# Kernel optimization log

Measured on AMD Instinct MI355X. Metric: run time of the kernel, lower is better.

## Reference

```python
import jax, jax.numpy as jnp
import numpy as np

N_NODES = 500_000
MEM_D = 128
MSG_D = 256  # stored messages have MSG_D + 1 columns (message + timestamp slot)
B = 200_000


def setup_inputs() -> dict:
    key = jax.random.key(0)
    k1, k2, k3, k4, k5, k6, k7 = jax.random.split(key, 7)
    memory = jax.random.normal(k1, (N_NODES, MEM_D), dtype=jnp.float32)
    last_update = jax.random.uniform(k2, (N_NODES,), dtype=jnp.float32)
    messages = jax.random.normal(k3, (N_NODES, MSG_D + 1), dtype=jnp.float32)
    node_id_to_messages = jax.random.normal(k4, (N_NODES, MSG_D + 1), dtype=jnp.float32)
    values = jax.random.normal(k5, (B, MEM_D), dtype=jnp.float32)
    node_idxs = jax.random.randint(k6, (B,), 0, N_NODES, dtype=jnp.int64 if jax.config.jax_enable_x64 else jnp.int32)
    nodes = jax.random.randint(k7, (B,), 0, N_NODES, dtype=jnp.int64 if jax.config.jax_enable_x64 else jnp.int32)
    return {
        "memory": memory,
        "last_update": last_update,
        "messages": messages,
        "node_id_to_messages": node_id_to_messages,
        "values": values,
        "node_idxs": node_idxs,
        "nodes": nodes,
    }


def reference(memory, last_update, messages, node_id_to_messages, values, node_idxs, nodes):
    # get_memory: row gather from persistent memory buffer
    mem_out = memory[node_idxs]                      # [B, MEM_D]
    # get_last_update: scalar gather
    lu_out = last_update[node_idxs]                  # [B]
    # set_memory: row scatter (index_copy) into memory buffer
    new_memory = memory.at[node_idxs].set(values)    # [N, MEM_D]
    # store_raw_messages: messages[nodes, :] = node_id_to_messages[nodes]
    new_messages = messages.at[nodes].set(node_id_to_messages[nodes])  # [N, MSG_D+1]
    return mem_out, lu_out, new_memory, new_messages
```

## Files before the change

### kernel.cpp

```cpp
#include <hip/hip_runtime.h>

#define N_NODES 500000
#define MEM_D   128
#define MSG_W   257
#define BATCH   200000

#define G_UNITS   6400000
#define M_UNITS   16000000
#define S_UNITS   32125000
#define GM_UNITS  22400000
#define TOTAL_UNITS 54525000

typedef float f4 __attribute__((ext_vector_type(4)));

__device__ __forceinline__ f4 nt_load4(const f4* p) {
    return __builtin_nontemporal_load(p);
}
__device__ __forceinline__ void nt_store4(f4* p, f4 v) {
    __builtin_nontemporal_store(v, p);
}

__global__ void init_kernel(int* __restrict__ winner,
                            unsigned int* __restrict__ flag32) {
    int i = blockIdx.x * blockDim.x + threadIdx.x;
    int stride = gridDim.x * blockDim.x;
    for (int j = i; j < N_NODES; j += stride) winner[j] = -1;
    for (int j = i; j < N_NODES / 4; j += stride) flag32[j] = 0u;
}

__global__ void scatter_idx_kernel(const int* __restrict__ node_idxs,
                                   const int* __restrict__ nodes,
                                   int* __restrict__ winner,
                                   unsigned char* __restrict__ flag) {
    int i = blockIdx.x * blockDim.x + threadIdx.x;
    int stride = gridDim.x * blockDim.x;
    for (; i < BATCH; i += stride) {
        atomicMax(&winner[node_idxs[i]], i);
        flag[nodes[i]] = 1;
    }
}

__global__ void fused_kernel(const float* __restrict__ memory,
                             const float* __restrict__ last_update,
                             const float* __restrict__ messages,
                             const float* __restrict__ nid2msg,
                             const float* __restrict__ values,
                             const int* __restrict__ node_idxs,
                             const int* __restrict__ winner,
                             const unsigned char* __restrict__ flag,
                             float* __restrict__ mem_out,
                             float* __restrict__ lu_out,
                             float* __restrict__ new_memory,
                             float* __restrict__ new_messages) {
    const f4* mem4 = reinterpret_cast<const f4*>(memory);
    const f4* val4 = reinterpret_cast<const f4*>(values);
    const f4* msg4 = reinterpret_cast<const f4*>(messages);
    const f4* src4 = reinterpret_cast<const f4*>(nid2msg);
    f4* memout4 = reinterpret_cast<f4*>(mem_out);
    f4* newmem4 = reinterpret_cast<f4*>(new_memory);
    f4* newmsg4 = reinterpret_cast<f4*>(new_messages);

    int i = blockIdx.x * blockDim.x + threadIdx.x;
    int stride = gridDim.x * blockDim.x;
    for (; i < TOTAL_UNITS; i += stride) {
        if (i < G_UNITS) {
            int row  = i >> 5;
            int col4 = i & 31;
            int idx  = node_idxs[row];
            f4 v = mem4[(long)idx * 32 + col4];
            nt_store4(&memout4[i], v);
            if (col4 == 0) {
                __builtin_nontemporal_store(last_update[idx], &lu_out[row]);
            }
        } else if (i < GM_UNITS) {
            int j    = i - G_UNITS;
            int row  = j >> 5;
            int col4 = j & 31;
            int w = winner[row];
            f4 v;
            if (w >= 0) {
                v = val4[(long)w * 32 + col4];
            } else {
                v = nt_load4(&mem4[j]);
            }
            nt_store4(&newmem4[j], v);
        } else {
            int j = i - GM_UNITS;
            int e  = j * 4;
            int r0 = e / 257;
            int r3 = (e + 3) / 257;
            if (r0 == r3) {
                f4 v;
                if (flag[r0]) {
                    v = nt_load4(&src4[j]);
                } else {
                    v = nt_load4(&msg4[j]);
                }
                nt_store4(&newmsg4[j], v);
            } else {
                #pragma unroll
                for (int k = 0; k < 4; ++k) {
                    int r = (e + k) / 257;
                    float v = (flag[r] ? nid2msg : messages)[e + k];
                    new_messages[e + k] = v;
                }
            }
        }
    }
}

extern "C" void kernel_launch(void* const* d_in, const int* in_sizes, int n_in,
                              void* d_out, int out_size, void* d_ws, size_t ws_size,
                              hipStream_t stream) {
    const float* memory       = (const float*)d_in[0];
    const float* last_update  = (const float*)d_in[1];
    const float* messages     = (const float*)d_in[2];
    const float* nid2msg      = (const float*)d_in[3];
    const float* values       = (const float*)d_in[4];
    const int*   node_idxs    = (const int*)d_in[5];
    const int*   nodes        = (const int*)d_in[6];

    float* out = (float*)d_out;
    float* mem_out      = out;
    float* lu_out       = out + (long)BATCH * MEM_D;
    float* new_memory   = lu_out + BATCH;
    float* new_messages = new_memory + (long)N_NODES * MEM_D;

    int* winner = (int*)d_ws;
    unsigned char* flag = (unsigned char*)d_ws + (size_t)N_NODES * sizeof(int);

    const int BS = 256;

    init_kernel<<<512, BS, 0, stream>>>(winner, (unsigned int*)flag);

    scatter_idx_kernel<<<(BATCH + BS - 1) / BS, BS, 0, stream>>>(
        node_idxs, nodes, winner, flag);

    fused_kernel<<<2048, BS, 0, stream>>>(memory, last_update, messages,
                                          nid2msg, values, node_idxs,
                                          winner, flag,
                                          mem_out, lu_out, new_memory,
                                          new_messages);
}
```

Baseline: 360.7 us.

## Split fused kernel into per-segment loops with 4-way unrolled batched loads

Replaces the single unified grid-stride loop, which branched per unit across three segments, with separate loops for the gather, memory scatter and message copy. Each loop issues four independent 16-byte loads before storing them, giving more memory-level parallelism per thread. The last_update gather moves into its own loop over batch rows. The cost is more registers per thread and extra tail-loop code.

Result: slower. 392.5 us (+8.8%).

```diff
diff --git a/kernel.cpp b/kernel.cpp
--- a/kernel.cpp
+++ b/kernel.cpp
@@ -5,11 +5,9 @@
 #define MSG_W   257
 #define BATCH   200000
 
-#define G_UNITS   6400000
-#define M_UNITS   16000000
-#define S_UNITS   32125000
-#define GM_UNITS  22400000
-#define TOTAL_UNITS 54525000
+#define G_UNITS 6400000
+#define M_UNITS 16000000
+#define S_UNITS 32125000
 
 typedef float f4 __attribute__((ext_vector_type(4)));
 
@@ -60,49 +58,101 @@
     f4* newmem4 = reinterpret_cast<f4*>(new_memory);
     f4* newmsg4 = reinterpret_cast<f4*>(new_messages);
 
-    int i = blockIdx.x * blockDim.x + threadIdx.x;
-    int stride = gridDim.x * blockDim.x;
-    for (; i < TOTAL_UNITS; i += stride) {
-        if (i < G_UNITS) {
-            int row  = i >> 5;
-            int col4 = i & 31;
-            int idx  = node_idxs[row];
-            f4 v = mem4[(long)idx * 32 + col4];
-            nt_store4(&memout4[i], v);
-            if (col4 == 0) {
-                __builtin_nontemporal_store(last_update[idx], &lu_out[row]);
+    const int tid = blockIdx.x * blockDim.x + threadIdx.x;
+    const int stride = gridDim.x * blockDim.x;
+
+    for (int r = tid; r < BATCH; r += stride) {
+        __builtin_nontemporal_store(last_update[node_idxs[r]], &lu_out[r]);
+    }
+
+    {
+        int i = tid;
+        for (; i + 3 * stride < G_UNITS; i += 4 * stride) {
+            f4 v[4];
+            #pragma unroll
+            for (int u = 0; u < 4; ++u) {
+                int ii = i + u * stride;
+                int idx = node_idxs[ii >> 5];
+                v[u] = mem4[(long)idx * 32 + (ii & 31)];
             }
-        } else if (i < GM_UNITS) {
-            int j    = i - G_UNITS;
-            int row  = j >> 5;
-            int col4 = j & 31;
-            int w = winner[row];
+            #pragma unroll
+            for (int u = 0; u < 4; ++u) nt_store4(&memout4[i + u * stride], v[u]);
+        }
+        for (; i < G_UNITS; i += stride) {
+            int idx = node_idxs[i >> 5];
+            nt_store4(&memout4[i], mem4[(long)idx * 32 + (i & 31)]);
+        }
+    }
+
+    {
+        int i = tid;
+        for (; i + 3 * stride < M_UNITS; i += 4 * stride) {
+            f4 v[4];
+            #pragma unroll
+            for (int u = 0; u < 4; ++u) {
+                int ii = i + u * stride;
+                int w = winner[ii >> 5];
+                if (w >= 0) v[u] = val4[(long)w * 32 + (ii & 31)];
+                else        v[u] = nt_load4(&mem4[ii]);
+            }
+            #pragma unroll
+            for (int u = 0; u < 4; ++u) nt_store4(&newmem4[i + u * stride], v[u]);
+        }
+        for (; i < M_UNITS; i += stride) {
+            int w = winner[i >> 5];
             f4 v;
-            if (w >= 0) {
-                v = val4[(long)w * 32 + col4];
-            } else {
-                v = nt_load4(&mem4[j]);
+            if (w >= 0) v = val4[(long)w * 32 + (i & 31)];
+            else        v = nt_load4(&mem4[i]);
+            nt_store4(&newmem4[i], v);
+        }
+    }
+
+    {
+        int i = tid;
+        for (; i + 3 * stride < S_UNITS; i += 4 * stride) {
+            f4 v[4];
+            int bnd[4];
+            #pragma unroll
+            for (int u = 0; u < 4; ++u) {
+                int ii = i + u * stride;
+                int e  = ii * 4;
+                int r0 = e / 257;
+                int r3 = (e + 3) / 257;
+                bnd[u] = (r0 != r3);
+                if (!bnd[u]) {
+                    if (flag[r0]) v[u] = nt_load4(&src4[ii]);
+                    else          v[u] = nt_load4(&msg4[ii]);
+                }
             }
-            nt_store4(&newmem4[j], v);
-        } else {
-            int j = i - GM_UNITS;
-            int e  = j * 4;
+            #pragma unroll
+            for (int u = 0; u < 4; ++u) {
+                int ii = i + u * stride;
+                if (!bnd[u]) {
+                    nt_store4(&newmsg4[ii], v[u]);
+                } else {
+                    int e = ii * 4;
+                    #pragma unroll
+                    for (int k = 0; k < 4; ++k) {
+                        int r = (e + k) / 257;
+                        new_messages[e + k] = (flag[r] ? nid2msg : messages)[e + k];
+                    }
+                }
+            }
+        }
+        for (; i < S_UNITS; i += stride) {
+            int e  = i * 4;
             int r0 = e / 257;
             int r3 = (e + 3) / 257;
             if (r0 == r3) {
                 f4 v;
-                if (flag[r0]) {
-                    v = nt_load4(&src4[j]);
-                } else {
-                    v = nt_load4(&msg4[j]);
-                }
-                nt_store4(&newmsg4[j], v);
+                if (flag[r0]) v = nt_load4(&src4[i]);
+                else          v = nt_load4(&msg4[i]);
+                nt_store4(&newmsg4[i], v);
             } else {
                 #pragma unroll
                 for (int k = 0; k < 4; ++k) {
                     int r = (e + k) / 257;
-                    float v = (flag[r] ? nid2msg : messages)[e + k];
-                    new_messages[e + k] = v;
+                    new_messages[e + k] = (flag[r] ? nid2msg : messages)[e + k];
                 }
             }
         }
```

## Partition fused kernel blocks statically across gather, memory-scatter and message tasks

Applied to the files above, without the earlier changes.

Replaces the single grid-stride loop over a concatenated unit space with block-range specialization: fixed block counts are dedicated to the gather, the new_memory copy and the messages copy, each looping over its own range. This removes per-iteration branch divergence across segments and lets all three streams run concurrently, with block counts roughly proportional to the bytes each task moves. The risk is load imbalance if the fixed split does not match actual bandwidth per task, since the gather segment does random reads.

Measured after the change: 373.5 us. 3.5% more time.

```diff
diff --git a/kernel.cpp b/kernel.cpp
--- a/kernel.cpp
+++ b/kernel.cpp
@@ -5,11 +5,14 @@
 #define MSG_W   257
 #define BATCH   200000
 
-#define G_UNITS   6400000
-#define M_UNITS   16000000
-#define S_UNITS   32125000
-#define GM_UNITS  22400000
-#define TOTAL_UNITS 54525000
+#define G_UNITS 6400000
+#define M_UNITS 16000000
+#define S_UNITS 32125000
+
+#define A_BLOCKS 240
+#define B_BLOCKS 601
+#define C_BLOCKS 1207
+#define BS 256
 
 typedef float f4 __attribute__((ext_vector_type(4)));
 
@@ -60,10 +63,12 @@
     f4* newmem4 = reinterpret_cast<f4*>(new_memory);
     f4* newmsg4 = reinterpret_cast<f4*>(new_messages);
 
-    int i = blockIdx.x * blockDim.x + threadIdx.x;
-    int stride = gridDim.x * blockDim.x;
-    for (; i < TOTAL_UNITS; i += stride) {
-        if (i < G_UNITS) {
+    const int b = blockIdx.x;
+
+    if (b < A_BLOCKS) {
+        const int stride = A_BLOCKS * BS;
+        int i = b * BS + threadIdx.x;
+        for (; i < G_UNITS; i += stride) {
             int row  = i >> 5;
             int col4 = i & 31;
             int idx  = node_idxs[row];
@@ -72,31 +77,37 @@
             if (col4 == 0) {
                 __builtin_nontemporal_store(last_update[idx], &lu_out[row]);
             }
-        } else if (i < GM_UNITS) {
-            int j    = i - G_UNITS;
-            int row  = j >> 5;
-            int col4 = j & 31;
+        }
+    } else if (b < A_BLOCKS + B_BLOCKS) {
+        const int stride = B_BLOCKS * BS;
+        int i = (b - A_BLOCKS) * BS + threadIdx.x;
+        for (; i < M_UNITS; i += stride) {
+            int row  = i >> 5;
+            int col4 = i & 31;
             int w = winner[row];
             f4 v;
             if (w >= 0) {
                 v = val4[(long)w * 32 + col4];
             } else {
-                v = nt_load4(&mem4[j]);
+                v = nt_load4(&mem4[i]);
             }
-            nt_store4(&newmem4[j], v);
-        } else {
-            int j = i - GM_UNITS;
-            int e  = j * 4;
+            nt_store4(&newmem4[i], v);
+        }
+    } else {
+        const int stride = C_BLOCKS * BS;
+        int i = (b - A_BLOCKS - B_BLOCKS) * BS + threadIdx.x;
+        for (; i < S_UNITS; i += stride) {
+            int e  = i * 4;
             int r0 = e / 257;
             int r3 = (e + 3) / 257;
             if (r0 == r3) {
                 f4 v;
                 if (flag[r0]) {
-                    v = nt_load4(&src4[j]);
+                    v = nt_load4(&src4[i]);
                 } else {
-                    v = nt_load4(&msg4[j]);
+                    v = nt_load4(&msg4[i]);
                 }
-                nt_store4(&newmsg4[j], v);
+                nt_store4(&newmsg4[i], v);
             } else {
                 #pragma unroll
                 for (int k = 0; k < 4; ++k) {
@@ -129,16 +140,12 @@
     int* winner = (int*)d_ws;
     unsigned char* flag = (unsigned char*)d_ws + (size_t)N_NODES * sizeof(int);
 
-    const int BS = 256;
-
     init_kernel<<<512, BS, 0, stream>>>(winner, (unsigned int*)flag);
 
     scatter_idx_kernel<<<(BATCH + BS - 1) / BS, BS, 0, stream>>>(
         node_idxs, nodes, winner, flag);
 
-    fused_kernel<<<2048, BS, 0, stream>>>(memory, last_update, messages,
-                                          nid2msg, values, node_idxs,
-                                          winner, flag,
-                                          mem_out, lu_out, new_memory,
-                                          new_messages);
+    fused_kernel<<<A_BLOCKS + B_BLOCKS + C_BLOCKS, BS, 0, stream>>>(
+        memory, last_update, messages, nid2msg, values, node_idxs,
+        winner, flag, mem_out, lu_out, new_memory, new_messages);
 }
```
